# Kernel tuning notes

Measured on AMD Instinct MI355X. Metric: run time of the kernel, lower is better.

The kernel has to match this reference:

```python
import jax, jax.numpy as jnp
import numpy as np

# dims: T time steps, B batch, CIN/COUT conv channels, HxW spatial, K kernel
T, B, CIN, COUT, H, Wd, K = 10, 32, 3, 64, 64, 64, 3
DECAY = 0.2      # LIF leak factor
INH = 1.625      # lateral inhibition strength (mode='threshold')


def setup_inputs() -> dict:
    key = jax.random.key(0)
    k1, k2 = jax.random.split(key)
    x = (jax.random.uniform(k1, (T, B, CIN, H, Wd)) < 0.2).astype(jnp.float32)
    W = jax.random.normal(k2, (COUT, CIN, K, K), dtype=jnp.float32)
    # normweight(): zero-mean, unit-std (biased) per output filter
    W = W - W.mean(axis=(1, 2, 3), keepdims=True)
    W = W / W.reshape(COUT, -1).std(axis=1).reshape(COUT, 1, 1, 1)
    return {"x": x, "W": W}


def _conv(x, W):
    # Conv2d stride=1, padding=1, no bias, NCHW/OIHW
    return jax.lax.conv_general_dilated(
        x, W, window_strides=(1, 1), padding=((1, 1), (1, 1)),
        dimension_numbers=("NCHW", "OIHW", "NCHW"))


def reference(x, W):
    def step(mem, x_t):
        i = _conv(x_t, W)                                        # (B,COUT,H,W)
        # ATB: adaptive per-channel threshold = max over batch+spatial
        thr = jnp.max(i, axis=(0, 2, 3), keepdims=True) + 1e-4   # (1,COUT,1,1)
        # ASF: clamp then thresholded sigmoid filter
        cur = jnp.maximum(i, 0.0)
        i_asf = thr * jax.nn.sigmoid((cur - 0.4 * thr) * (8.0 / thr))
        # LIF update with threshold = thr (set by ATB)
        mem = mem * DECAY + i_asf
        s = (mem > thr).astype(mem.dtype)                        # spikes 0/1
        # WTA k=1: keep only the strongest spiking channel per location
        score = mem * s
        winner = jnp.argmax(score, axis=1)                       # (B,H,W)
        oh = jnp.moveaxis(jax.nn.one_hot(winner, COUT, dtype=mem.dtype), -1, 1)
        s = s * oh
        # membrane reset of fired neurons
        mem = mem * (1.0 - s)
        # lateral inhibition: suppress non-winners at spiking locations
        any_sp = jnp.max(s, axis=1, keepdims=True)
        mem = mem - INH * thr * any_sp * (1.0 - s)
        return mem, s

    mem0 = jnp.zeros((B, COUT, H, Wd), jnp.float32)
    _, spikes = jax.lax.scan(step, mem0, x)
    return spikes  # (T,B,COUT,H,W)
```

## Files before the change

### kernel.cpp

```cpp
#include <hip/hip_runtime.h>
#include <math.h>

#define TT 10
#define BB 32
#define CIN 3
#define COUT 64
#define HH 64
#define WW 64
#define HW (HH*WW)
#define DECAY 0.2f
#define INH 1.625f

#define ISLAB ((size_t)HW * COUT)

__device__ __forceinline__ unsigned int enc_f(float f) {
    unsigned int u = __float_as_uint(f);
    return (u & 0x80000000u) ? ~u : (u | 0x80000000u);
}
__device__ __forceinline__ float dec_f(unsigned int u) {
    u = (u & 0x80000000u) ? (u & 0x7FFFFFFFu) : ~u;
    return __uint_as_float(u);
}

__global__ __launch_bounds__(256) void conv_kernel(
    const float* __restrict__ x,
    const float* __restrict__ Wt,
    float* __restrict__ ibuf,
    unsigned int* __restrict__ thr_raw,
    int t0)
{
    __shared__ float sx[CIN][6][68];
    __shared__ float wmax[4][COUT];

    const int tid  = threadIdx.x;
    const int lane = tid & 63;
    const int wave = tid >> 6;
    const int h0   = blockIdx.x * 4;
    const int b    = blockIdx.y;
    const int t    = t0 + blockIdx.z;

    float w[27];
    #pragma unroll
    for (int k = 0; k < 27; k++) w[k] = Wt[lane * 27 + k];

    const float* xb = x + ((size_t)t * BB + b) * (CIN * HW);
    for (int l = tid; l < CIN * 6 * 66; l += 256) {
        int ci  = l / 396;
        int r   = (l % 396) / 66;
        int col = l % 66;
        int gh = h0 + r - 1;
        int gw = col - 1;
        float v = 0.f;
        if (gh >= 0 && gh < HH && gw >= 0 && gw < WW)
            v = xb[ci * HW + gh * WW + gw];
        sx[ci][r][col] = v;
    }
    __syncthreads();

    const int h = h0 + wave;
    float* ist = ibuf + ((size_t)blockIdx.z * BB + b) * ISLAB
                      + (size_t)h * WW * COUT;

    float mx = -INFINITY;

    for (int cc = 0; cc < 16; cc++) {
        float acc0 = 0.f, acc1 = 0.f, acc2 = 0.f, acc3 = 0.f;
        #pragma unroll
        for (int ci = 0; ci < CIN; ci++)
            #pragma unroll
            for (int kh = 0; kh < 3; kh++) {
                const float* rp = &sx[ci][wave + kh][cc * 4];
                float4 q = *(const float4*)rp;
                float2 r2 = *(const float2*)(rp + 4);
                float x0 = q.x, x1 = q.y, x2 = q.z, x3 = q.w;
                float x4 = r2.x, x5 = r2.y;
                const float w0 = w[ci * 9 + kh * 3 + 0];
                const float w1 = w[ci * 9 + kh * 3 + 1];
                const float w2 = w[ci * 9 + kh * 3 + 2];
                acc0 = fmaf(w0, x0, acc0); acc0 = fmaf(w1, x1, acc0); acc0 = fmaf(w2, x2, acc0);
                acc1 = fmaf(w0, x1, acc1); acc1 = fmaf(w1, x2, acc1); acc1 = fmaf(w2, x3, acc1);
                acc2 = fmaf(w0, x2, acc2); acc2 = fmaf(w1, x3, acc2); acc2 = fmaf(w2, x4, acc2);
                acc3 = fmaf(w0, x3, acc3); acc3 = fmaf(w1, x4, acc3); acc3 = fmaf(w2, x5, acc3);
            }
        mx = fmaxf(mx, fmaxf(fmaxf(acc0, acc1), fmaxf(acc2, acc3)));
        ist[(size_t)(cc * 4 + 0) * COUT + lane] = acc0;
        ist[(size_t)(cc * 4 + 1) * COUT + lane] = acc1;
        ist[(size_t)(cc * 4 + 2) * COUT + lane] = acc2;
        ist[(size_t)(cc * 4 + 3) * COUT + lane] = acc3;
    }

    wmax[wave][lane] = mx;
    __syncthreads();
    if (wave == 0) {
        float m = fmaxf(fmaxf(wmax[0][lane], wmax[1][lane]),
                        fmaxf(wmax[2][lane], wmax[3][lane]));
        atomicMax(&thr_raw[t * COUT + lane], enc_f(m));
    }
}

__global__ __launch_bounds__(256) void lif_kernel(
    const float* __restrict__ ibuf,
    const unsigned int* __restrict__ thr_raw,
    float* __restrict__ out,
    float* __restrict__ memws,
    int t0, int nt)
{
    const int tid  = threadIdx.x;
    const int lane = tid & 63;
    const int p0   = __builtin_amdgcn_readfirstlane((tid >> 6) * 16);
    const int b    = blockIdx.x >> 6;
    const int h    = blockIdx.x & 63;

    float* mrow = memws + ((size_t)b * HH + h) * WW * COUT;

    float mem[16];
    if (t0 == 0) {
        #pragma unroll
        for (int j = 0; j < 16; j++) mem[j] = 0.f;
    } else {
        #pragma unroll
        for (int j = 0; j < 16; j++)
            mem[j] = mrow[(size_t)(p0 + j) * COUT + lane];
    }

    #pragma unroll 1
    for (int tt = 0; tt < nt; tt++) {
        const int t = t0 + tt;
        const float* ild = ibuf + ((size_t)tt * BB + b) * ISLAB
                                + (size_t)h * WW * COUT;
        float* os = out + (((size_t)t * BB + b) * COUT) * HW + h * WW;

        #pragma unroll
        for (int g = 0; g < 4; g++) {
            int c  = g * 16 + (tid >> 4);
            int w4 = (tid & 15) * 4;
            *(float4*)(os + (size_t)c * HW + w4) = make_float4(0.f, 0.f, 0.f, 0.f);
        }

        float thr   = dec_f(thr_raw[t * COUT + lane]) + 1e-4f;
        float sinv  = 8.0f / thr;
        float s04   = 0.4f * thr;
        float sinh_ = INH * thr;

        int fmask = 0;

        #pragma unroll
        for (int j = 0; j < 16; j++) {
            float iv  = ild[(size_t)(p0 + j) * COUT + lane];
            float cur = fmaxf(iv, 0.f);
            float z   = (cur - s04) * sinv;
            float sig = 1.0f / (1.0f + expf(-z));
            float m   = mem[j] * DECAY + thr * sig;
            int   sp  = m > thr;
            float score = sp ? m : 0.f;

            unsigned long long blt = __ballot(sp);
            int fr = 0, sp_any = 0;
            if (blt) {
                float bs = score;
                int   bc = lane;
                #pragma unroll
                for (int off = 32; off > 0; off >>= 1) {
                    float so = __shfl_xor(bs, off, 64);
                    int   co = __shfl_xor(bc, off, 64);
                    if (so > bs || (so == bs && co < bc)) { bs = so; bc = co; }
                }
                int spw = __shfl(sp, bc, 64);
                fr     = (lane == bc) && sp;
                sp_any = spw;
            }
            mem[j] = fr ? 0.f : (m - (sp_any ? sinh_ : 0.f));
            if (fr) fmask |= (1 << j);
        }

        __syncthreads();

        if (fmask) {
            #pragma unroll
            for (int j = 0; j < 16; j++)
                if (fmask & (1 << j))
                    os[(size_t)lane * HW + p0 + j] = 1.0f;
        }
        __syncthreads();
    }

    if (t0 + nt < TT) {
        #pragma unroll
        for (int j = 0; j < 16; j++)
            mrow[(size_t)(p0 + j) * COUT + lane] = mem[j];
    }
}

extern "C" void kernel_launch(void* const* d_in, const int* in_sizes, int n_in,
                              void* d_out, int out_size, void* d_ws, size_t ws_size,
                              hipStream_t stream) {
    const float* x = (const float*)d_in[0];
    const float* W = (const float*)d_in[1];
    float* out     = (float*)d_out;

    char* ws = (char*)d_ws;
    unsigned int* thr = (unsigned int*)ws;
    const size_t IOFF   = 65536;
    const size_t SLABB  = ISLAB * sizeof(float);

    hipMemsetAsync(thr, 0, TT * COUT * sizeof(unsigned int), stream);

    if (ws_size >= IOFF + TT * SLABB) {
        float* ibuf = (float*)(ws + IOFF);
        conv_kernel<<<dim3(HH / 4, BB, TT), 256, 0, stream>>>(x, W, ibuf, thr, 0);
        lif_kernel<<<dim3(BB * HH), 256, 0, stream>>>(ibuf, thr, out,
                                                      (float*)(ws + IOFF), 0, TT);
    } else {
        float* ibuf  = (float*)(ws + IOFF);
        float* memws = (float*)(ws + IOFF + SLABB);
        for (int t = 0; t < TT; t++) {
            conv_kernel<<<dim3(HH / 4, BB, 1), 256, 0, stream>>>(x, W, ibuf, thr, t);
            lif_kernel<<<dim3(BB * HH), 256, 0, stream>>>(ibuf, thr, out,
                                                          memws, t, 1);
        }
    }
}
```

Measured before the change: 545.4 us.

## Recompute convolution inside LIF kernel instead of materializing conv output buffer

The conv pass now only computes per-channel maxima for the adaptive thresholds and no longer writes the full conv output (T×B×HW×COUT floats) to workspace. The LIF kernel recomputes the 3x3 convolution per row from a small shared-memory input tile and feeds the results straight into the LIF/WTA update. This removes a large global write and read of the intermediate buffer, and the now-unused memory-state spill path, at the cost of doing the convolution twice.

Measured after the change: 532.6 us. 2.4% less time.

```diff
diff --git a/kernel.cpp b/kernel.cpp
--- a/kernel.cpp
+++ b/kernel.cpp
@@ -11,8 +11,6 @@
 #define DECAY 0.2f
 #define INH 1.625f
 
-#define ISLAB ((size_t)HW * COUT)
-
 __device__ __forceinline__ unsigned int enc_f(float f) {
     unsigned int u = __float_as_uint(f);
     return (u & 0x80000000u) ? ~u : (u | 0x80000000u);
@@ -22,12 +20,10 @@
     return __uint_as_float(u);
 }
 
-__global__ __launch_bounds__(256) void conv_kernel(
+__global__ __launch_bounds__(256) void thr_kernel(
     const float* __restrict__ x,
     const float* __restrict__ Wt,
-    float* __restrict__ ibuf,
-    unsigned int* __restrict__ thr_raw,
-    int t0)
+    unsigned int* __restrict__ thr_raw)
 {
     __shared__ float sx[CIN][6][68];
     __shared__ float wmax[4][COUT];
@@ -37,7 +33,7 @@
     const int wave = tid >> 6;
     const int h0   = blockIdx.x * 4;
     const int b    = blockIdx.y;
-    const int t    = t0 + blockIdx.z;
+    const int t    = blockIdx.z;
 
     float w[27];
     #pragma unroll
@@ -56,10 +52,6 @@
         sx[ci][r][col] = v;
     }
     __syncthreads();
-
-    const int h = h0 + wave;
-    float* ist = ibuf + ((size_t)blockIdx.z * BB + b) * ISLAB
-                      + (size_t)h * WW * COUT;
 
     float mx = -INFINITY;
 
@@ -83,10 +75,6 @@
                 acc3 = fmaf(w0, x3, acc3); acc3 = fmaf(w1, x4, acc3); acc3 = fmaf(w2, x5, acc3);
             }
         mx = fmaxf(mx, fmaxf(fmaxf(acc0, acc1), fmaxf(acc2, acc3)));
-        ist[(size_t)(cc * 4 + 0) * COUT + lane] = acc0;
-        ist[(size_t)(cc * 4 + 1) * COUT + lane] = acc1;
-        ist[(size_t)(cc * 4 + 2) * COUT + lane] = acc2;
-        ist[(size_t)(cc * 4 + 3) * COUT + lane] = acc3;
     }
 
     wmax[wave][lane] = mx;
@@ -98,36 +86,44 @@
     }
 }
 
-__global__ __launch_bounds__(256) void lif_kernel(
-    const float* __restrict__ ibuf,
+__global__ __launch_bounds__(256) void fused_kernel(
+    const float* __restrict__ x,
+    const float* __restrict__ Wt,
     const unsigned int* __restrict__ thr_raw,
-    float* __restrict__ out,
-    float* __restrict__ memws,
-    int t0, int nt)
+    float* __restrict__ out)
 {
+    __shared__ float sx[CIN][3][68];
+
     const int tid  = threadIdx.x;
     const int lane = tid & 63;
-    const int p0   = __builtin_amdgcn_readfirstlane((tid >> 6) * 16);
+    const int wave = tid >> 6;
+    const int p0   = __builtin_amdgcn_readfirstlane(wave * 16);
     const int b    = blockIdx.x >> 6;
     const int h    = blockIdx.x & 63;
 
-    float* mrow = memws + ((size_t)b * HH + h) * WW * COUT;
+    float w[27];
+    #pragma unroll
+    for (int k = 0; k < 27; k++) w[k] = Wt[lane * 27 + k];
 
     float mem[16];
-    if (t0 == 0) {
-        #pragma unroll
-        for (int j = 0; j < 16; j++) mem[j] = 0.f;
-    } else {
-        #pragma unroll
-        for (int j = 0; j < 16; j++)
-            mem[j] = mrow[(size_t)(p0 + j) * COUT + lane];
-    }
+    #pragma unroll
+    for (int j = 0; j < 16; j++) mem[j] = 0.f;
 
     #pragma unroll 1
-    for (int tt = 0; tt < nt; tt++) {
-        const int t = t0 + tt;
-        const float* ild = ibuf + ((size_t)tt * BB + b) * ISLAB
-                                + (size_t)h * WW * COUT;
+    for (int t = 0; t < TT; t++) {
+        const float* xb = x + ((size_t)t * BB + b) * (CIN * HW);
+        for (int l = tid; l < CIN * 3 * 66; l += 256) {
+            int ci  = l / 198;
+            int r   = (l % 198) / 66;
+            int col = l % 66;
+            int gh = h + r - 1;
+            int gw = col - 1;
+            float v = 0.f;
+            if (gh >= 0 && gh < HH && gw >= 0 && gw < WW)
+                v = xb[ci * HW + gh * WW + gw];
+            sx[ci][r][col] = v;
+        }
+
         float* os = out + (((size_t)t * BB + b) * COUT) * HW + h * WW;
 
         #pragma unroll
@@ -137,6 +133,8 @@
             *(float4*)(os + (size_t)c * HW + w4) = make_float4(0.f, 0.f, 0.f, 0.f);
         }
 
+        __syncthreads();
+
         float thr   = dec_f(thr_raw[t * COUT + lane]) + 1e-4f;
         float sinv  = 8.0f / thr;
         float s04   = 0.4f * thr;
@@ -144,36 +142,59 @@
 
         int fmask = 0;
 
+#define LIF_PX(J, ACC) {                                                    \
+        float cur = fmaxf(ACC, 0.f);                                        \
+        float z   = (cur - s04) * sinv;                                     \
+        float sig = 1.0f / (1.0f + expf(-z));                               \
+        float m   = mem[J] * DECAY + thr * sig;                             \
+        int   sp  = m > thr;                                                \
+        float score = sp ? m : 0.f;                                         \
+        unsigned long long blt = __ballot(sp);                              \
+        int fr = 0, sp_any = 0;                                             \
+        if (blt) {                                  \
+            float bs = score;                                               \
+            int   bc = lane;                                                \
+            _Pragma("unroll")                                               \
+            for (int off = 32; off > 0; off >>= 1) {                        \
+                float so = __shfl_xor(bs, off, 64);                         \
+                int   co = __shfl_xor(bc, off, 64);                         \
+                if (so > bs || (so == bs && co < bc)) { bs = so; bc = co; } \
+            }                                                               \
+            int spw = __shfl(sp, bc, 64);      \
+            fr     = (lane == bc) && sp;                                    \
+            sp_any = spw;                                                   \
+        }                                                                   \
+        mem[J] = fr ? 0.f : (m - (sp_any ? sinh_ : 0.f));                   \
+        if (fr) fmask |= (1 << (J));                                        \
+    }
+
         #pragma unroll
-        for (int j = 0; j < 16; j++) {
-            float iv  = ild[(size_t)(p0 + j) * COUT + lane];
-            float cur = fmaxf(iv, 0.f);
-            float z   = (cur - s04) * sinv;
-            float sig = 1.0f / (1.0f + expf(-z));
-            float m   = mem[j] * DECAY + thr * sig;
-            int   sp  = m > thr;
-            float score = sp ? m : 0.f;
-
-            unsigned long long blt = __ballot(sp);
-            int fr = 0, sp_any = 0;
-            if (blt) {
-                float bs = score;
-                int   bc = lane;
+        for (int ch = 0; ch < 4; ch++) {
+            const int c0 = p0 + ch * 4;
+            float acc0 = 0.f, acc1 = 0.f, acc2 = 0.f, acc3 = 0.f;
+            #pragma unroll
+            for (int ci = 0; ci < CIN; ci++)
                 #pragma unroll
-                for (int off = 32; off > 0; off >>= 1) {
-                    float so = __shfl_xor(bs, off, 64);
-                    int   co = __shfl_xor(bc, off, 64);
-                    if (so > bs || (so == bs && co < bc)) { bs = so; bc = co; }
+                for (int kh = 0; kh < 3; kh++) {
+                    const float* rp = &sx[ci][kh][c0];
+                    float4 q = *(const float4*)rp;
+                    float2 r2 = *(const float2*)(rp + 4);
+                    float x0 = q.x, x1 = q.y, x2 = q.z, x3 = q.w;
+                    float x4 = r2.x, x5 = r2.y;
+                    const float w0 = w[ci * 9 + kh * 3 + 0];
+                    const float w1 = w[ci * 9 + kh * 3 + 1];
+                    const float w2 = w[ci * 9 + kh * 3 + 2];
+                    acc0 = fmaf(w0, x0, acc0); acc0 = fmaf(w1, x1, acc0); acc0 = fmaf(w2, x2, acc0);
+                    acc1 = fmaf(w0, x1, acc1); acc1 = fmaf(w1, x2, acc1); acc1 = fmaf(w2, x3, acc1);
+                    acc2 = fmaf(w0, x2, acc2); acc2 = fmaf(w1, x3, acc2); acc2 = fmaf(w2, x4, acc2);
+                    acc3 = fmaf(w0, x3, acc3); acc3 = fmaf(w1, x4, acc3); acc3 = fmaf(w2, x5, acc3);
                 }
-                int spw = __shfl(sp, bc, 64);
-                fr     = (lane == bc) && sp;
-                sp_any = spw;
-            }
-            mem[j] = fr ? 0.f : (m - (sp_any ? sinh_ : 0.f));
-            if (fr) fmask |= (1 << j);
-        }
-
-        __syncthreads();
+            LIF_PX(ch * 4 + 0, acc0);
+            LIF_PX(ch * 4 + 1, acc1);
+            LIF_PX(ch * 4 + 2, acc2);
+            LIF_PX(ch * 4 + 3, acc3);
+        }
+#undef LIF_PX
 
         if (fmask) {
             #pragma unroll
@@ -182,12 +203,6 @@
                     os[(size_t)lane * HW + p0 + j] = 1.0f;
         }
         __syncthreads();
-    }
-
-    if (t0 + nt < TT) {
-        #pragma unroll
-        for (int j = 0; j < 16; j++)
-            mrow[(size_t)(p0 + j) * COUT + lane] = mem[j];
     }
 }
 
@@ -198,25 +213,9 @@
     const float* W = (const float*)d_in[1];
     float* out     = (float*)d_out;
 
-    char* ws = (char*)d_ws;
-    unsigned int* thr = (unsigned int*)ws;
-    const size_t IOFF   = 65536;
-    const size_t SLABB  = ISLAB * sizeof(float);
-
+    unsigned int* thr = (unsigned int*)d_ws;
     hipMemsetAsync(thr, 0, TT * COUT * sizeof(unsigned int), stream);
 
-    if (ws_size >= IOFF + TT * SLABB) {
-        float* ibuf = (float*)(ws + IOFF);
-        conv_kernel<<<dim3(HH / 4, BB, TT), 256, 0, stream>>>(x, W, ibuf, thr, 0);
-        lif_kernel<<<dim3(BB * HH), 256, 0, stream>>>(ibuf, thr, out,
-                                                      (float*)(ws + IOFF), 0, TT);
-    } else {
-        float* ibuf  = (float*)(ws + IOFF);
-        float* memws = (float*)(ws + IOFF + SLABB);
-        for (int t = 0; t < TT; t++) {
-            conv_kernel<<<dim3(HH / 4, BB, 1), 256, 0, stream>>>(x, W, ibuf, thr, t);
-            lif_kernel<<<dim3(BB * HH), 256, 0, stream>>>(ibuf, thr, out,
-                                                          memws, t, 1);
-        }
-    }
-}
+    thr_kernel<<<dim3(HH / 4, BB, TT), 256, 0, stream>>>(x, W, thr);
+    fused_kernel<<<dim3(BB * HH), 256, 0, stream>>>(x, W, thr, out);
+}
```
